# Performance work log

Measured on AMD Instinct MI355X. Metric: run time of the kernel, lower is better.

Reference implementation:

```python
import jax, jax.numpy as jnp
import numpy as np

NUM_BITS = 8  # byte_size default used by HilbertFlatten.forward -> hilbert_flatten(x)


def _hilbert_flat_indices(shape, num_bits=NUM_BITS):
    """Flat (raveled) source index for each position along the Hilbert curve.

    Vectorized Skilling-style decode, matching numpy-hilbert-curve's decode():
    hilbert ints 0..N-1 -> D-dim coords, then ravel to flat gather indices.
    Data-independent: depends only on the array shape.
    """
    num_dims = len(shape)
    n = int(np.prod(shape))
    nb_total = num_dims * num_bits
    s = np.arange(n, dtype=np.uint64)
    # Unpack bits MSB-first: (n, num_dims*num_bits). Done column-wise to avoid a
    # huge uint64 intermediate.
    bits = np.empty((n, nb_total), dtype=bool)
    for j in range(nb_total):
        shift = np.uint64(nb_total - 1 - j)
        bits[:, j] = (s >> shift) & np.uint64(1)
    # binary -> gray:  g = h ^ (h >> 1)
    gray = bits.copy()
    gray[:, 1:] ^= bits[:, :-1]
    # De-interleave: (n, num_bits, num_dims) -> (n, num_dims, num_bits)
    gray = np.swapaxes(gray.reshape(n, num_bits, num_dims), 1, 2).copy()
    # Undo the encode transforms: iterate backwards through bits and dims.
    for bit in range(num_bits - 1, -1, -1):
        for dim in range(num_dims - 1, -1, -1):
            mask = gray[:, dim, bit][:, None]
            # Where bit is on: invert dim-0 lower bits.
            gray[:, 0, bit + 1:] ^= mask
            # Where bit is off: swap lower bits of dim with dim 0.
            to_flip = ~mask & (gray[:, 0, bit + 1:] ^ gray[:, dim, bit + 1:])
            gray[:, dim, bit + 1:] ^= to_flip
            gray[:, 0, bit + 1:] ^= to_flip
    # Pack bit-planes back to integer coordinates: (n, num_dims)
    pows = (1 << np.arange(num_bits - 1, -1, -1)).astype(np.int64)
    locs = (gray.astype(np.int64) * pows).sum(-1)
    return np.ravel_multi_index(tuple(locs.T), shape)


def setup_inputs() -> dict:
    key = jax.random.key(0)
    x = jax.random.normal(key, (256, 256, 256), dtype=jnp.float32)
    return {"x": x}


def reference(x):
    # hilbert_flatten: out[s] = x[decode(s)] for s in 0..N-1  ->  1-D array of N
    perm = jnp.asarray(_hilbert_flat_indices(tuple(x.shape)))
    return jnp.take(x.reshape(-1), perm)
```

## Files before the change

### kernel.cpp

```cpp
#include <hip/hip_runtime.h>


typedef __attribute__((address_space(1))) const void global_cvoid;
typedef __attribute__((address_space(3))) void lds_void;

__global__ __launch_bounds__(256) void hilbert_lds_kernel(
    const float* __restrict__ x, float* __restrict__ out, unsigned ngroups) {
    __shared__ float lds[4 * 512];

    unsigned nb = blockIdx.x;
    unsigned cpx = gridDim.x >> 3;
    unsigned b = (nb & 7u) * cpx + (nb >> 3);
    unsigned tid = threadIdx.x;
    unsigned gid = b * 256u + tid;
    if (gid >= ngroups) return;
    unsigned S = gid << 3;
    unsigned lane = tid & 63u;
    unsigned wave = tid >> 6;

    unsigned g = S ^ (S >> 1);
    unsigned G[3];
#pragma unroll
    for (int d = 0; d < 3; ++d) {
        unsigned v = (g >> (2 - d)) & 0x00249249u;
        v = (v ^ (v >> 2)) & 0x030C30C3u;
        v = (v ^ (v >> 4)) & 0x0300F00Fu;
        v = (v ^ (v >> 8)) & 0x000000FFu;
        G[d] = v;
    }
    G[0] |= 0x100u;
    G[1] |= 0x200u;
    G[2] |= 0x400u;
#pragma unroll
    for (int bit = 6; bit >= 0; --bit) {
        const unsigned low = ((1u << (7 - bit)) - 1u) | 0x0F00u;
#pragma unroll
        for (int dim = 2; dim >= 0; --dim) {
            unsigned m = (G[dim] >> (7 - bit)) & 1u;
            unsigned diff = (G[0] ^ G[dim]) & low;
            unsigned t = diff & (m - 1u);
            G[0] ^= ((0u - m) & low) ^ t;
            G[dim] ^= t;
        }
    }
    unsigned s3m = 0u - ((S >> 3) & 1u);
    unsigned V0 = (0xF0u ^ s3m) & 0xFFu;
    const unsigned V1 = 0x3Cu, V2 = 0x66u;
    unsigned B[3];
#pragma unroll
    for (int d = 0; d < 3; ++d) {
        unsigned cd = 0u - ((G[d] >> 11) & 1u);
        unsigned a0 = (0u - ((G[d] >> 8) & 1u)) ^ cd;
        unsigned a1 = (0u - ((G[d] >> 9) & 1u)) ^ cd;
        unsigned a2 = (0u - ((G[d] >> 10) & 1u)) ^ cd;
        B[d] = ((a0 & V0) ^ (a1 & V1) ^ (a2 & V2) ^ cd) & 0xFFu;
    }
    unsigned baseflat = ((G[0] & 0xFEu) << 16) | ((G[1] & 0xFEu) << 8)
                      | (G[2] & 0xFEu);

    unsigned regionflat = baseflat & 0x00F8F8F8u;
    const float* gbase = x + regionflat;
    unsigned dxl = lane >> 4;
    unsigned dyl = (lane >> 1) & 7u;
    unsigned half = lane & 1u;
    auto lds3 = (__attribute__((address_space(3))) float*)lds;
#pragma unroll
    for (unsigned h = 0; h < 2; ++h) {
        const float* src = gbase + (h * 4u + dxl) * 65536u + dyl * 256u + half * 4u;
        __builtin_amdgcn_global_load_lds((global_cvoid*)src,
                                         (lds_void*)(lds3 + wave * 512u + h * 256u),
                                         16, 0, 0);
    }
    asm volatile("s_waitcnt vmcnt(0)" ::: "memory");

    unsigned bx = (baseflat >> 16) & 6u;
    unsigned by = (baseflat >> 8) & 6u;
    unsigned bz = baseflat & 6u;
    unsigned bxp = (bx >> 1) & 1u;
    unsigned byp = (by >> 1) & 1u;
    const float* lw = lds + wave * 512u;
    unsigned i0 = byp,      j0 = bxp;
    unsigned i1 = byp,      j1 = bxp ^ 1u;
    unsigned i2 = byp ^ 1u, j2 = bxp;
    unsigned i3 = byp ^ 1u, j3 = bxp ^ 1u;
    float2 r0 = *(const float2*)&lw[(bx + i0) * 64u + (by + j0) * 8u + bz];
    float2 r1 = *(const float2*)&lw[(bx + i1) * 64u + (by + j1) * 8u + bz];
    float2 r2 = *(const float2*)&lw[(bx + i2) * 64u + (by + j2) * 8u + bz];
    float2 r3 = *(const float2*)&lw[(bx + i3) * 64u + (by + j3) * 8u + bz];
    bool sx = bxp != 0u, sy = byp != 0u;
    float2 a0 = sx ? r1 : r0;
    float2 a1 = sx ? r0 : r1;
    float2 a2 = sx ? r3 : r2;
    float2 a3 = sx ? r2 : r3;
    float2 q00 = sy ? a2 : a0;
    float2 q01 = sy ? a3 : a1;
    float2 q10 = sy ? a0 : a2;
    float2 q11 = sy ? a1 : a3;

    float out8[8];
#pragma unroll
    for (int rr = 0; rr < 8; ++rr) {
        unsigned f0 = (B[0] >> rr) & 1u;
        unsigned f1 = (B[1] >> rr) & 1u;
        unsigned f2 = (B[2] >> rr) & 1u;
        float2 t0 = f1 ? q01 : q00;
        float2 t1 = f1 ? q11 : q10;
        float2 t  = f0 ? t1 : t0;
        out8[rr] = f2 ? t.y : t.x;
    }
    float4* o4 = (float4*)(out + S);
    o4[0] = make_float4(out8[0], out8[1], out8[2], out8[3]);
    o4[1] = make_float4(out8[4], out8[5], out8[6], out8[7]);
}

extern "C" void kernel_launch(void* const* d_in, const int* in_sizes, int n_in,
                              void* d_out, int out_size, void* d_ws, size_t ws_size,
                              hipStream_t stream) {
    const float* x = (const float*)d_in[0];
    float* out = (float*)d_out;
    unsigned n = (unsigned)out_size;
    unsigned ngroups = n >> 3;
    unsigned blocks = (ngroups + 255u) / 256u;
    hilbert_lds_kernel<<<blocks, 256, 0, stream>>>(x, out, ngroups);
}
```

Measured before the change: 26.22 us.

## Process two 512-element regions per wave with shuffled coalesced nontemporal stores

Each wave now handles 1024 consecutive output elements as two 512-element cubes, issuing four async global-to-LDS loads before one wait. This doubles memory-level parallelism per wave and halves the grid. Outputs are rearranged with cross-lane shuffles so every lane writes contiguous 16-byte chunks covering 256-element spans, using nontemporal stores. The costs are more shuffle instructions, more registers and LDS per block, and the bounds check is dropped, so the size must be a multiple of 4096.

```diff
diff --git a/kernel.cpp b/kernel.cpp
--- a/kernel.cpp
+++ b/kernel.cpp
@@ -1,23 +1,12 @@
 #include <hip/hip_runtime.h>
 
 
+typedef float f32x4 __attribute__((ext_vector_type(4)));
 typedef __attribute__((address_space(1))) const void global_cvoid;
 typedef __attribute__((address_space(3))) void lds_void;
 
-__global__ __launch_bounds__(256) void hilbert_lds_kernel(
-    const float* __restrict__ x, float* __restrict__ out, unsigned ngroups) {
-    __shared__ float lds[4 * 512];
-
-    unsigned nb = blockIdx.x;
-    unsigned cpx = gridDim.x >> 3;
-    unsigned b = (nb & 7u) * cpx + (nb >> 3);
-    unsigned tid = threadIdx.x;
-    unsigned gid = b * 256u + tid;
-    if (gid >= ngroups) return;
-    unsigned S = gid << 3;
-    unsigned lane = tid & 63u;
-    unsigned wave = tid >> 6;
-
+__device__ __forceinline__ void decode8(unsigned S, unsigned B[3],
+                                        unsigned& baseflat) {
     unsigned g = S ^ (S >> 1);
     unsigned G[3];
 #pragma unroll
@@ -28,9 +17,7 @@
         v = (v ^ (v >> 8)) & 0x000000FFu;
         G[d] = v;
     }
-    G[0] |= 0x100u;
-    G[1] |= 0x200u;
-    G[2] |= 0x400u;
+    G[0] |= 0x100u; G[1] |= 0x200u; G[2] |= 0x400u;
 #pragma unroll
     for (int bit = 6; bit >= 0; --bit) {
         const unsigned low = ((1u << (7 - bit)) - 1u) | 0x0F00u;
@@ -46,7 +33,6 @@
     unsigned s3m = 0u - ((S >> 3) & 1u);
     unsigned V0 = (0xF0u ^ s3m) & 0xFFu;
     const unsigned V1 = 0x3Cu, V2 = 0x66u;
-    unsigned B[3];
 #pragma unroll
     for (int d = 0; d < 3; ++d) {
         unsigned cd = 0u - ((G[d] >> 11) & 1u);
@@ -55,62 +41,101 @@
         unsigned a2 = (0u - ((G[d] >> 10) & 1u)) ^ cd;
         B[d] = ((a0 & V0) ^ (a1 & V1) ^ (a2 & V2) ^ cd) & 0xFFu;
     }
-    unsigned baseflat = ((G[0] & 0xFEu) << 16) | ((G[1] & 0xFEu) << 8)
-                      | (G[2] & 0xFEu);
+    baseflat = ((G[0] & 0xFEu) << 16) | ((G[1] & 0xFEu) << 8) | (G[2] & 0xFEu);
+}
 
-    unsigned regionflat = baseflat & 0x00F8F8F8u;
-    const float* gbase = x + regionflat;
+__global__ __launch_bounds__(256) void hilbert_r2_kernel(
+    const float* __restrict__ x, float* __restrict__ out) {
+    __shared__ float lds[4 * 1024];
+    unsigned nb = blockIdx.x;
+    unsigned cpx = gridDim.x >> 3;
+    unsigned b = (nb & 7u) * cpx + (nb >> 3);
+    unsigned tid = threadIdx.x;
+    unsigned lane = tid & 63u;
+    unsigned wave = tid >> 6;
+    unsigned W = b * 4u + wave;
+    unsigned Sw = W * 1024u;
+
+    unsigned B0[3], B1[3], bf0, bf1;
+    decode8(Sw + lane * 8u, B0, bf0);
+    decode8(Sw + 512u + lane * 8u, B1, bf1);
+
     unsigned dxl = lane >> 4;
     unsigned dyl = (lane >> 1) & 7u;
     unsigned half = lane & 1u;
     auto lds3 = (__attribute__((address_space(3))) float*)lds;
+    unsigned rf0 = bf0 & 0x00F8F8F8u;
+    unsigned rf1 = bf1 & 0x00F8F8F8u;
 #pragma unroll
-    for (unsigned h = 0; h < 2; ++h) {
-        const float* src = gbase + (h * 4u + dxl) * 65536u + dyl * 256u + half * 4u;
-        __builtin_amdgcn_global_load_lds((global_cvoid*)src,
-                                         (lds_void*)(lds3 + wave * 512u + h * 256u),
-                                         16, 0, 0);
+    for (unsigned q = 0; q < 2; ++q) {
+        const float* gbase = x + (q ? rf1 : rf0);
+#pragma unroll
+        for (unsigned h = 0; h < 2; ++h) {
+            const float* src = gbase + (h * 4u + dxl) * 65536u
+                             + dyl * 256u + half * 4u;
+            __builtin_amdgcn_global_load_lds(
+                (global_cvoid*)src,
+                (lds_void*)(lds3 + wave * 1024u + q * 512u + h * 256u),
+                16, 0, 0);
+        }
     }
     asm volatile("s_waitcnt vmcnt(0)" ::: "memory");
 
-    unsigned bx = (baseflat >> 16) & 6u;
-    unsigned by = (baseflat >> 8) & 6u;
-    unsigned bz = baseflat & 6u;
-    unsigned bxp = (bx >> 1) & 1u;
-    unsigned byp = (by >> 1) & 1u;
-    const float* lw = lds + wave * 512u;
-    unsigned i0 = byp,      j0 = bxp;
-    unsigned i1 = byp,      j1 = bxp ^ 1u;
-    unsigned i2 = byp ^ 1u, j2 = bxp;
-    unsigned i3 = byp ^ 1u, j3 = bxp ^ 1u;
-    float2 r0 = *(const float2*)&lw[(bx + i0) * 64u + (by + j0) * 8u + bz];
-    float2 r1 = *(const float2*)&lw[(bx + i1) * 64u + (by + j1) * 8u + bz];
-    float2 r2 = *(const float2*)&lw[(bx + i2) * 64u + (by + j2) * 8u + bz];
-    float2 r3 = *(const float2*)&lw[(bx + i3) * 64u + (by + j3) * 8u + bz];
-    bool sx = bxp != 0u, sy = byp != 0u;
-    float2 a0 = sx ? r1 : r0;
-    float2 a1 = sx ? r0 : r1;
-    float2 a2 = sx ? r3 : r2;
-    float2 a3 = sx ? r2 : r3;
-    float2 q00 = sy ? a2 : a0;
-    float2 q01 = sy ? a3 : a1;
-    float2 q10 = sy ? a0 : a2;
-    float2 q11 = sy ? a1 : a3;
+#pragma unroll
+    for (unsigned q = 0; q < 2; ++q) {
+        unsigned baseflat = q ? bf1 : bf0;
+        const unsigned* B = q ? B1 : B0;
+        unsigned bx = (baseflat >> 16) & 6u;
+        unsigned by = (baseflat >> 8) & 6u;
+        unsigned bz = baseflat & 6u;
+        unsigned bxp = (bx >> 1) & 1u;
+        unsigned byp = (by >> 1) & 1u;
+        const float* lw = lds + wave * 1024u + q * 512u;
+        float2 r0 = *(const float2*)&lw[(bx + byp) * 64u + (by + bxp) * 8u + bz];
+        float2 r1 = *(const float2*)&lw[(bx + byp) * 64u + (by + (bxp ^ 1u)) * 8u + bz];
+        float2 r2 = *(const float2*)&lw[(bx + (byp ^ 1u)) * 64u + (by + bxp) * 8u + bz];
+        float2 r3 = *(const float2*)&lw[(bx + (byp ^ 1u)) * 64u + (by + (bxp ^ 1u)) * 8u + bz];
+        bool sx = bxp != 0u, sy = byp != 0u;
+        float2 a0 = sx ? r1 : r0;
+        float2 a1 = sx ? r0 : r1;
+        float2 a2 = sx ? r3 : r2;
+        float2 a3 = sx ? r2 : r3;
+        float2 q00 = sy ? a2 : a0;
+        float2 q01 = sy ? a3 : a1;
+        float2 q10 = sy ? a0 : a2;
+        float2 q11 = sy ? a1 : a3;
 
-    float out8[8];
+        float o8[8];
 #pragma unroll
-    for (int rr = 0; rr < 8; ++rr) {
-        unsigned f0 = (B[0] >> rr) & 1u;
-        unsigned f1 = (B[1] >> rr) & 1u;
-        unsigned f2 = (B[2] >> rr) & 1u;
-        float2 t0 = f1 ? q01 : q00;
-        float2 t1 = f1 ? q11 : q10;
-        float2 t  = f0 ? t1 : t0;
-        out8[rr] = f2 ? t.y : t.x;
+        for (int rr = 0; rr < 8; ++rr) {
+            unsigned f0 = (B[0] >> rr) & 1u;
+            unsigned f1 = (B[1] >> rr) & 1u;
+            unsigned f2 = (B[2] >> rr) & 1u;
+            float2 t0 = f1 ? q01 : q00;
+            float2 t1 = f1 ? q11 : q10;
+            float2 t  = f0 ? t1 : t0;
+            o8[rr] = f2 ? t.y : t.x;
+        }
+
+        int src1 = (int)(lane >> 1);
+        int src2 = (int)(32u + (lane >> 1));
+        bool hi = (lane & 1u) != 0u;
+        float vA[4], vB[4];
+#pragma unroll
+        for (int j = 0; j < 4; ++j) {
+            float a = __shfl(o8[j], src1, 64);
+            float bb = __shfl(o8[4 + j], src1, 64);
+            vA[j] = hi ? bb : a;
+            float c = __shfl(o8[j], src2, 64);
+            float d = __shfl(o8[4 + j], src2, 64);
+            vB[j] = hi ? d : c;
+        }
+        unsigned WB = Sw + q * 512u;
+        __builtin_nontemporal_store((f32x4){vA[0], vA[1], vA[2], vA[3]},
+                                    (f32x4*)(out + WB + 4u * lane));
+        __builtin_nontemporal_store((f32x4){vB[0], vB[1], vB[2], vB[3]},
+                                    (f32x4*)(out + WB + 256u + 4u * lane));
     }
-    float4* o4 = (float4*)(out + S);
-    o4[0] = make_float4(out8[0], out8[1], out8[2], out8[3]);
-    o4[1] = make_float4(out8[4], out8[5], out8[6], out8[7]);
 }
 
 extern "C" void kernel_launch(void* const* d_in, const int* in_sizes, int n_in,
@@ -119,7 +144,7 @@
     const float* x = (const float*)d_in[0];
     float* out = (float*)d_out;
     unsigned n = (unsigned)out_size;
-    unsigned ngroups = n >> 3;
-    unsigned blocks = (ngroups + 255u) / 256u;
-    hilbert_lds_kernel<<<blocks, 256, 0, stream>>>(x, out, ngroups);
+    unsigned nwaves = n / 1024u;
+    unsigned blocks = nwaves / 4u;
+    hilbert_r2_kernel<<<blocks, 256, 0, stream>>>(x, out);
 }
```

New measurement: 26.61 us. No clear change (+1.5%).
